# Kernel optimization log

Hardware: AMD Instinct MI355X
Metric: run time of the kernel (lower is better)

The kernel has to match this reference:

```python
import jax, jax.numpy as jnp
import numpy as np


def _quantize(mat):
    # per-row (last-dim) symmetric int8 quantization; scale stored in fp16 like torch
    max_val = (jnp.max(jnp.abs(mat), axis=-1) / 127.0).astype(jnp.float16)
    # torch's .to(int8) truncates toward zero; jnp astype does the same for in-range values
    q = (mat / max_val[..., None].astype(mat.dtype)).astype(jnp.int8)
    return q, max_val


def setup_inputs() -> dict:
    key = jax.random.key(0)
    k1, k2, k3, k4 = jax.random.split(key, 4)
    B, S, D_IN, D_OUT = 4, 2048, 4096, 4096
    x = jax.random.normal(k1, (B, S, D_IN), dtype=jnp.float32)
    origin_weight = jax.random.normal(k2, (D_OUT, D_IN), dtype=jnp.float32) * 0.02
    bias = jax.random.normal(k3, (D_OUT,), dtype=jnp.float32) * 0.01
    act_max = jax.random.normal(k4, (D_IN,), dtype=jnp.float32)
    return {"x": x, "origin_weight": origin_weight, "bias": bias,
            "act_max": act_max, "alpha": 32}


def reference(x, origin_weight, bias, act_max, alpha):
    d_in = act_max.shape[-1]
    # get_unq_idx_topk: top-alpha outlier channels by |act_max|
    _, idx = jax.lax.top_k(jnp.abs(act_max), alpha)          # [alpha]
    t = jnp.ones((d_in,), dtype=origin_weight.dtype).at[idx].set(0)

    # weight decomposition + quantization (done in __init__ in torch)
    weight_q, w_max = _quantize(origin_weight * t)           # [out,in] int8, [out] fp16
    weight_unq = origin_weight[:, idx].T                      # [alpha, out]

    # activation decomposition + per-token quantization
    x_unq = x[..., idx]                                       # [B,S,alpha]
    x_q, x_max = _quantize(x * t.astype(x.dtype))             # [B,S,in] int8, [B,S] fp16

    # simulated MatMulInteger: int8 values multiplied in fp32
    res_q = jnp.matmul(x_q.astype(jnp.float32), weight_q.T.astype(jnp.float32))  # [B,S,out]
    mx = (x_max[..., None] * w_max[None, :]).astype(jnp.float32)                  # [B,S,out]
    res_q = (res_q * mx).astype(x.dtype)

    # fp outlier path
    res_unq = jnp.matmul(x_unq, weight_unq) + bias
    return res_q + res_unq
```

## Files before the change

### kernel.cpp

```cpp
#include <hip/hip_runtime.h>
#include <hip/hip_fp16.h>

typedef __attribute__((ext_vector_type(4)))  int   i32x4;
typedef __attribute__((ext_vector_type(16))) int   i32x16;

#define ALPHA 32
#define BM 256
#define BN 128
#define BK 64


__global__ __launch_bounds__(256) void topk_kernel(const float* __restrict__ act_max,
                                                   int* __restrict__ idx_out,
                                                   unsigned* __restrict__ tbits,
                                                   int K) {
  __shared__ float v[4096];
  __shared__ float rv[4];
  __shared__ int   ri[4];
  __shared__ unsigned bits[128];
  const int t = threadIdx.x;
  for (int i = t; i < K; i += 256) v[i] = fabsf(act_max[i]);
  for (int i = t; i < K / 32; i += 256) bits[i] = 0xFFFFFFFFu;
  __syncthreads();
  for (int sel = 0; sel < ALPHA; ++sel) {
    float bv = -1.f; int bi = 0;
    for (int i = t; i < K; i += 256) {
      float x = v[i];
      if (x > bv) { bv = x; bi = i; }
    }
    for (int m = 1; m < 64; m <<= 1) {
      float ov = __shfl_xor(bv, m);
      int   oi = __shfl_xor(bi, m);
      if (ov > bv || (ov == bv && oi < bi)) { bv = ov; bi = oi; }
    }
    if ((t & 63) == 0) { rv[t >> 6] = bv; ri[t >> 6] = bi; }
    __syncthreads();
    if (t == 0) {
      for (int u = 1; u < 4; ++u)
        if (rv[u] > bv || (rv[u] == bv && ri[u] < bi)) { bv = rv[u]; bi = ri[u]; }
      idx_out[sel] = bi;
      v[bi] = -2.f;
      bits[bi >> 5] &= ~(1u << (bi & 31));
    }
    __syncthreads();
  }
  for (int i = t; i < K / 32; i += 256) tbits[i] = bits[i];
}

__global__ __launch_bounds__(1024) void quant_panel_kernel(
    const float* __restrict__ srcW, const float* __restrict__ srcX,
    const unsigned* __restrict__ tbits, const int* __restrict__ idx,
    signed char* __restrict__ wq, signed char* __restrict__ xq,
    _Float16* __restrict__ wmax, _Float16* __restrict__ xmax,
    float* __restrict__ wuf, float* __restrict__ xuf,
    int npw, int K, int N, int M) {
  const int t = threadIdx.x;
  const int b = blockIdx.x;
  const float* src; signed char* q; _Float16* smax; float* unq; int r0, R;
  if (b < npw) { src = srcW; q = wq; smax = wmax; unq = wuf; r0 = b * 32; R = N; }
  else         { src = srcX; q = xq; smax = xmax; unq = xuf; r0 = (b - npw) * 32; R = M; }
  __shared__ unsigned bits[128];
  __shared__ float wred[8][16];
  __shared__ float scs[8];
  __shared__ signed char qt[8 * 4096];
  const int lane = t & 63, w = t >> 6;
  for (int i = t; i < K / 32; i += 1024) bits[i] = tbits[i];
  __syncthreads();
  const int k0 = t * 4;
  const unsigned bw = bits[k0 >> 5] >> (k0 & 31);
  const bool m0 = bw & 1u, m1 = bw & 2u, m2 = bw & 4u, m3 = bw & 8u;
  const size_t pbase = (size_t)r0 * K;
  for (int g = 0; g < 4; ++g) {
    float4 v[8];
#pragma unroll
    for (int i = 0; i < 8; ++i) {
      float4 x = ((const float4*)(src + (size_t)(r0 + g * 8 + i) * K))[t];
      if (!m0) x.x = 0.f; if (!m1) x.y = 0.f; if (!m2) x.z = 0.f; if (!m3) x.w = 0.f;
      v[i] = x;
      float am = fmaxf(fmaxf(fabsf(x.x), fabsf(x.y)), fmaxf(fabsf(x.z), fabsf(x.w)));
#pragma unroll
      for (int m = 1; m < 64; m <<= 1) am = fmaxf(am, __shfl_xor(am, m));
      if (lane == 0) wred[i][w] = am;
    }
    __syncthreads();
    if (t < 8) {
      float am = wred[t][0];
#pragma unroll
      for (int u = 1; u < 16; ++u) am = fmaxf(am, wred[t][u]);
      _Float16 sh = (_Float16)(am / 127.0f);
      scs[t] = (float)sh;
      smax[r0 + g * 8 + t] = sh;
    }
    __syncthreads();
    const int cc = t >> 2, sub = (t & 3) * 4;
#pragma unroll
    for (int i = 0; i < 8; ++i) {
      const float s = scs[i];
      char4 c;
      c.x = (signed char)(v[i].x / s);
      c.y = (signed char)(v[i].y / s);
      c.z = (signed char)(v[i].z / s);
      c.w = (signed char)(v[i].w / s);
      *(char4*)(qt + cc * 128 + ((i ^ (cc & 7)) << 4) + sub) = c;
    }
    __syncthreads();
#pragma unroll
    for (int i = 0; i < 2; ++i) {
      const int l = i * 1024 + t;
      const int c2 = l >> 3, rl = l & 7;
      int4 d = *(const int4*)(qt + c2 * 128 + ((rl ^ (c2 & 7)) << 4));
      *(int4*)(q + pbase + (size_t)c2 * 512 + (size_t)((g * 8 + rl) << 4)) = d;
    }
    __syncthreads();
  }
  {
    const int j = t >> 5, rl = t & 31;
    unq[(size_t)j * R + r0 + rl] = src[(size_t)(r0 + rl) * K + idx[j]];
  }
}

__device__ __forceinline__ void gld_lds16(const signed char* g, signed char* l) {
  __builtin_amdgcn_global_load_lds(
      (const __attribute__((address_space(1))) void*)g,
      (__attribute__((address_space(3))) void*)l, 16, 0, 0);
}

__global__ __launch_bounds__(256, 2) void gemm_kernel(
    const signed char* __restrict__ xq, const signed char* __restrict__ wq,
    const _Float16* __restrict__ xmax, const _Float16* __restrict__ wmax,
    const float* __restrict__ xuf,
    const float* __restrict__ wuf,
    const float* __restrict__ bias,
    float* __restrict__ out, int M, int N, int K) {
  __shared__ union {
    struct { signed char A[2][BM * BK]; signed char B[2][BN * BK]; } g;
    struct { float xu[ALPHA * BM]; float wu[ALPHA * BN]; } e;
  } sm;
  __shared__ _Float16 xmh[BM];
  __shared__ _Float16 wmh[BN];
  __shared__ float    bl[BN];

  const int t = threadIdx.x;
  const int bid = blockIdx.y * gridDim.x + blockIdx.x;
  const int xcd = bid & 7, loc = bid >> 3;
  const int bxi = xcd * 4 + (loc & 3);
  const int byi = loc >> 2;
  const int bm0 = byi * BM;
  const int bn0 = bxi * BN;
  const int lane = t & 63, w = t >> 6;
  const int wm = w >> 1, wn = w & 1;
  const int hi = lane >> 5, l31 = lane & 31;

  i32x16 acc[4][2] = {};

  const int tp = t >> 7;
  const int to = (t & 127) * 16;
  const signed char* aS = xq + (size_t)bm0 * K + (size_t)tp * 32 * K + to;
  const signed char* bS = wq + (size_t)bn0 * K + (size_t)tp * 32 * K + to;
  signed char* const aD = &sm.g.A[0][0] + t * 16;
  signed char* const bD = &sm.g.B[0][0] + t * 16;
  const size_t PSTR = (size_t)64 * K;

  auto STAGE = [&](int buf, int kt) {
    const size_t ko = (size_t)kt * 2048;
#pragma unroll
    for (int i = 0; i < 4; ++i)
      gld_lds16(aS + (size_t)i * PSTR + ko, aD + buf * (BM * BK) + i * 4096);
#pragma unroll
    for (int i = 0; i < 2; ++i)
      gld_lds16(bS + (size_t)i * PSTR + ko, bD + buf * (BN * BK) + i * 4096);
  };

  STAGE(0, 0);
  const int NT = K >> 6;
  const signed char* const aR0 = &sm.g.A[0][0] + (wm * 4) * 2048 + 16 * lane;
  const signed char* const bR0 = &sm.g.B[0][0] + (wn * 2) * 2048 + 16 * lane;

  for (int kt = 0; kt < NT; ++kt) {
    const int cur = kt & 1;
    asm volatile("s_waitcnt vmcnt(0)" ::: "memory");
    asm volatile("s_barrier" ::: "memory");
    const signed char* aRd = aR0 + cur * (BM * BK);
    const signed char* bRd = bR0 + cur * (BN * BK);
    i32x4 af[2][4], bf[2][2];
#pragma unroll
    for (int ks = 0; ks < 2; ++ks) {
#pragma unroll
      for (int mi = 0; mi < 4; ++mi) af[ks][mi] = *(const i32x4*)(aRd + mi * 2048 + ks * 1024);
#pragma unroll
      for (int ni = 0; ni < 2; ++ni) bf[ks][ni] = *(const i32x4*)(bRd + ni * 2048 + ks * 1024);
    }
    if (kt + 1 < NT) STAGE(cur ^ 1, kt + 1);
    __builtin_amdgcn_s_setprio(1);
#pragma unroll
    for (int ks = 0; ks < 2; ++ks)
#pragma unroll
      for (int mi = 0; mi < 4; ++mi)
#pragma unroll
        for (int ni = 0; ni < 2; ++ni)
          acc[mi][ni] = __builtin_amdgcn_mfma_i32_32x32x32_i8(af[ks][mi], bf[ks][ni], acc[mi][ni], 0, 0, 0);
    __builtin_amdgcn_s_setprio(0);
  }

  __syncthreads();
  {
    const float4* xs = (const float4*)xuf;
    float4* xl = (float4*)sm.e.xu;
#pragma unroll
    for (int i = 0; i < 8; ++i) {
      int p = i * 256 + t;
      int j = p >> 6, r4 = p & 63;
      xl[p] = xs[(size_t)j * (M >> 2) + (bm0 >> 2) + r4];
    }
    const float4* wsrc = (const float4*)wuf;
    float4* wl = (float4*)sm.e.wu;
#pragma unroll
    for (int i = 0; i < 4; ++i) {
      int p = i * 256 + t;
      int j = p >> 5, r4 = p & 31;
      wl[p] = wsrc[(size_t)j * (N >> 2) + (bn0 >> 2) + r4];
    }
    if (t < BM / 2) ((unsigned*)xmh)[t] = ((const unsigned*)(xmax + bm0))[t];
    if (t < BN / 2) ((unsigned*)wmh)[t] = ((const unsigned*)(wmax + bn0))[t];
    if (t < BN / 4) ((float4*)bl)[t] = ((const float4*)(bias + bn0))[t];
  }
  __syncthreads();

  const int c0 = wn * 64 + l31;
  const _Float16 wh0 = wmh[c0], wh1 = wmh[c0 + 32];
  const float bv0 = bl[c0], bv1 = bl[c0 + 32];
  const float* xul = sm.e.xu;
  const float* wul = sm.e.wu;

#pragma unroll
  for (int mi = 0; mi < 4; ++mi) {
    const int rbase = wm * 128 + mi * 32 + 4 * hi;
    float f0[16], f1[16];
#pragma unroll
    for (int r = 0; r < 16; ++r) {
      int row = rbase + (r & 3) + 8 * (r >> 2);
      _Float16 xh = xmh[row];
      float mx0 = (float)(_Float16)(xh * wh0);
      float mx1 = (float)(_Float16)(xh * wh1);
      f0[r] = (float)acc[mi][0][r] * mx0 + bv0;
      f1[r] = (float)acc[mi][1][r] * mx1 + bv1;
    }
#pragma unroll 4
    for (int j = 0; j < ALPHA; ++j) {
      const float4* xrow4 = (const float4*)(xul + j * BM + rbase);
      float wv0 = wul[j * BN + c0];
      float wv1 = wul[j * BN + c0 + 32];
#pragma unroll
      for (int gq = 0; gq < 4; ++gq) {
        float4 xv = xrow4[gq * 2];
        f0[gq * 4 + 0] += xv.x * wv0;  f1[gq * 4 + 0] += xv.x * wv1;
        f0[gq * 4 + 1] += xv.y * wv0;  f1[gq * 4 + 1] += xv.y * wv1;
        f0[gq * 4 + 2] += xv.z * wv0;  f1[gq * 4 + 2] += xv.z * wv1;
        f0[gq * 4 + 3] += xv.w * wv0;  f1[gq * 4 + 3] += xv.w * wv1;
      }
    }
#pragma unroll
    for (int r = 0; r < 16; ++r) {
      int row = bm0 + rbase + (r & 3) + 8 * (r >> 2);
      size_t o = (size_t)row * N + bn0;
      out[o + c0] = f0[r];
      out[o + c0 + 32] = f1[r];
    }
  }
}

extern "C" void kernel_launch(void* const* d_in, const int* in_sizes, int n_in,
                              void* d_out, int out_size, void* d_ws, size_t ws_size,
                              hipStream_t stream) {
  const float* x       = (const float*)d_in[0];
  const float* W       = (const float*)d_in[1];
  const float* bias    = (const float*)d_in[2];
  const float* act_max = (const float*)d_in[3];
  const int K = in_sizes[3];
  const int N = in_sizes[1] / K;
  const int M = in_sizes[0] / K;
  float* out = (float*)d_out;

  char* ws = (char*)d_ws;
  size_t off = 0;
  auto take = [&](size_t b) { char* p = ws + off; off += (b + 255) & ~(size_t)255; return p; };
  signed char* wq  = (signed char*)take((size_t)N * K);
  signed char* xq  = (signed char*)take((size_t)M * K);
  _Float16* wmax   = (_Float16*)take((size_t)N * 2);
  _Float16* xmax   = (_Float16*)take((size_t)M * 2);
  float* wuf       = (float*)take((size_t)ALPHA * N * 4);
  float* xuf       = (float*)take((size_t)ALPHA * M * 4);
  int* idx         = (int*)take(ALPHA * 4);
  unsigned* tbits  = (unsigned*)take((size_t)(K / 32) * 4);

  const int npw = N / 32, npx = M / 32;
  topk_kernel<<<1, 256, 0, stream>>>(act_max, idx, tbits, K);
  quant_panel_kernel<<<npw + npx, 1024, 0, stream>>>(W, x, tbits, idx, wq, xq,
                                                     wmax, xmax, wuf, xuf, npw, K, N, M);
  dim3 grid(N / BN, M / BM);
  gemm_kernel<<<grid, 256, 0, stream>>>(xq, wq, xmax, wmax, xuf, wuf, bias, out, M, N, K);
}
```

Measured before the change: 315.6 us.

## Use triple-buffered GEMM prefetch and 8-row quantization blocks

The GEMM mainloop now keeps three LDS stages, prefetching two k-tiles ahead with a partial vmcnt wait, so global-to-LDS loads overlap further with the MFMA work. The quantization kernel is restructured to 256-thread blocks handling 8 rows each, with one wave per row doing a wave-only max reduction. This removes the cross-wave reductions and extra barriers and launches many more blocks. The cost is more LDS per GEMM block (three stages of A and B), which may limit the intended two blocks per CU.

```diff
diff --git a/kernel.cpp b/kernel.cpp
--- a/kernel.cpp
+++ b/kernel.cpp
@@ -47,75 +47,70 @@
   for (int i = t; i < K / 32; i += 256) tbits[i] = bits[i];
 }
 
-__global__ __launch_bounds__(1024) void quant_panel_kernel(
+__global__ __launch_bounds__(256) void quant8_kernel(
     const float* __restrict__ srcW, const float* __restrict__ srcX,
-    const unsigned* __restrict__ tbits, const int* __restrict__ idx,
+    const unsigned* __restrict__ tbits, const int* __restrict__ idxg,
     signed char* __restrict__ wq, signed char* __restrict__ xq,
     _Float16* __restrict__ wmax, _Float16* __restrict__ xmax,
     float* __restrict__ wuf, float* __restrict__ xuf,
-    int npw, int K, int N, int M) {
-  const int t = threadIdx.x;
+    int nbw, int K, int N, int M) {
+  const int t = threadIdx.x, lane = t & 63, w = t >> 6;
   const int b = blockIdx.x;
   const float* src; signed char* q; _Float16* smax; float* unq; int r0, R;
-  if (b < npw) { src = srcW; q = wq; smax = wmax; unq = wuf; r0 = b * 32; R = N; }
-  else         { src = srcX; q = xq; smax = xmax; unq = xuf; r0 = (b - npw) * 32; R = M; }
+  if (b < nbw) { src = srcW; q = wq; smax = wmax; unq = wuf; r0 = b * 8; R = N; }
+  else         { src = srcX; q = xq; smax = xmax; unq = xuf; r0 = (b - nbw) * 8; R = M; }
   __shared__ unsigned bits[128];
-  __shared__ float wred[8][16];
-  __shared__ float scs[8];
   __shared__ signed char qt[8 * 4096];
-  const int lane = t & 63, w = t >> 6;
-  for (int i = t; i < K / 32; i += 1024) bits[i] = tbits[i];
-  __syncthreads();
-  const int k0 = t * 4;
-  const unsigned bw = bits[k0 >> 5] >> (k0 & 31);
-  const bool m0 = bw & 1u, m1 = bw & 2u, m2 = bw & 4u, m3 = bw & 8u;
-  const size_t pbase = (size_t)r0 * K;
-  for (int g = 0; g < 4; ++g) {
-    float4 v[8];
-#pragma unroll
-    for (int i = 0; i < 8; ++i) {
-      float4 x = ((const float4*)(src + (size_t)(r0 + g * 8 + i) * K))[t];
-      if (!m0) x.x = 0.f; if (!m1) x.y = 0.f; if (!m2) x.z = 0.f; if (!m3) x.w = 0.f;
-      v[i] = x;
-      float am = fmaxf(fmaxf(fabsf(x.x), fabsf(x.y)), fmaxf(fabsf(x.z), fabsf(x.w)));
-#pragma unroll
-      for (int m = 1; m < 64; m <<= 1) am = fmaxf(am, __shfl_xor(am, m));
-      if (lane == 0) wred[i][w] = am;
-    }
-    __syncthreads();
-    if (t < 8) {
-      float am = wred[t][0];
-#pragma unroll
-      for (int u = 1; u < 16; ++u) am = fmaxf(am, wred[t][u]);
-      _Float16 sh = (_Float16)(am / 127.0f);
-      scs[t] = (float)sh;
-      smax[r0 + g * 8 + t] = sh;
-    }
-    __syncthreads();
-    const int cc = t >> 2, sub = (t & 3) * 4;
-#pragma unroll
-    for (int i = 0; i < 8; ++i) {
-      const float s = scs[i];
+  for (int i = t; i < 128; i += 256) bits[i] = tbits[i];
+  __syncthreads();
+  const int shft = (lane & 7) * 4;
+#pragma unroll
+  for (int g = 0; g < 2; ++g) {
+    const int rl = w + 4 * g;
+    const float4* srow = (const float4*)(src + (size_t)(r0 + rl) * K);
+    float4 v[16];
+    float am = 0.f;
+#pragma unroll
+    for (int j = 0; j < 16; ++j) {
+      float4 x = srow[j * 64 + lane];
+      unsigned b4 = bits[j * 8 + (lane >> 3)] >> shft;
+      if (!(b4 & 1u)) x.x = 0.f;
+      if (!(b4 & 2u)) x.y = 0.f;
+      if (!(b4 & 4u)) x.z = 0.f;
+      if (!(b4 & 8u)) x.w = 0.f;
+      v[j] = x;
+      am = fmaxf(am, fmaxf(fmaxf(fabsf(x.x), fabsf(x.y)), fmaxf(fabsf(x.z), fabsf(x.w))));
+    }
+#pragma unroll
+    for (int m = 1; m < 64; m <<= 1) am = fmaxf(am, __shfl_xor(am, m));
+    const _Float16 sh = (_Float16)(am / 127.0f);
+    const float s = (float)sh;
+    if (lane == 0) smax[r0 + rl] = sh;
+    signed char* row = qt + rl * 4096;
+#pragma unroll
+    for (int j = 0; j < 16; ++j) {
+      float4 x = v[j];
       char4 c;
-      c.x = (signed char)(v[i].x / s);
-      c.y = (signed char)(v[i].y / s);
-      c.z = (signed char)(v[i].z / s);
-      c.w = (signed char)(v[i].w / s);
-      *(char4*)(qt + cc * 128 + ((i ^ (cc & 7)) << 4) + sub) = c;
-    }
-    __syncthreads();
-#pragma unroll
-    for (int i = 0; i < 2; ++i) {
-      const int l = i * 1024 + t;
-      const int c2 = l >> 3, rl = l & 7;
-      int4 d = *(const int4*)(qt + c2 * 128 + ((rl ^ (c2 & 7)) << 4));
-      *(int4*)(q + pbase + (size_t)c2 * 512 + (size_t)((g * 8 + rl) << 4)) = d;
-    }
-    __syncthreads();
+      c.x = (signed char)(x.x / s);
+      c.y = (signed char)(x.y / s);
+      c.z = (signed char)(x.z / s);
+      c.w = (signed char)(x.w / s);
+      const int c2 = j * 16 + (lane >> 2);
+      *(char4*)(row + ((c2 ^ rl) << 4) + (lane & 3) * 4) = c;
+    }
+  }
+  __syncthreads();
+  const size_t pbase = (size_t)(r0 >> 5) * 32 * K + (size_t)(r0 & 31) * 16;
+#pragma unroll
+  for (int i = 0; i < 8; ++i) {
+    const int s2 = i * 256 + t;
+    const int c2 = s2 >> 3, rl = s2 & 7;
+    int4 d = *(const int4*)(qt + rl * 4096 + ((c2 ^ rl) << 4));
+    *(int4*)(q + pbase + (size_t)c2 * 512 + rl * 16) = d;
   }
   {
-    const int j = t >> 5, rl = t & 31;
-    unq[(size_t)j * R + r0 + rl] = src[(size_t)(r0 + rl) * K + idx[j]];
+    const int j = t >> 3, rl = t & 7;
+    unq[(size_t)j * R + r0 + rl] = src[(size_t)(r0 + rl) * K + idxg[j]];
   }
 }
 
@@ -133,7 +128,7 @@
     const float* __restrict__ bias,
     float* __restrict__ out, int M, int N, int K) {
   __shared__ union {
-    struct { signed char A[2][BM * BK]; signed char B[2][BN * BK]; } g;
+    struct { signed char A[3][BM * BK]; signed char B[3][BN * BK]; } g;
     struct { float xu[ALPHA * BM]; float wu[ALPHA * BN]; } e;
   } sm;
   __shared__ _Float16 xmh[BM];
@@ -171,13 +166,40 @@
       gld_lds16(bS + (size_t)i * PSTR + ko, bD + buf * (BN * BK) + i * 4096);
   };
 
+  const int NT = K >> 6;
   STAGE(0, 0);
-  const int NT = K >> 6;
+  STAGE(1, 1);
   const signed char* const aR0 = &sm.g.A[0][0] + (wm * 4) * 2048 + 16 * lane;
   const signed char* const bR0 = &sm.g.B[0][0] + (wn * 2) * 2048 + 16 * lane;
 
-  for (int kt = 0; kt < NT; ++kt) {
-    const int cur = kt & 1;
+  int cur = 0, st = 2;
+  for (int kt = 0; kt < NT - 1; ++kt) {
+    asm volatile("s_waitcnt vmcnt(6)" ::: "memory");
+    asm volatile("s_barrier" ::: "memory");
+    const signed char* aRd = aR0 + cur * (BM * BK);
+    const signed char* bRd = bR0 + cur * (BN * BK);
+    i32x4 af[2][4], bf[2][2];
+#pragma unroll
+    for (int ks = 0; ks < 2; ++ks) {
+#pragma unroll
+      for (int mi = 0; mi < 4; ++mi) af[ks][mi] = *(const i32x4*)(aRd + mi * 2048 + ks * 1024);
+#pragma unroll
+      for (int ni = 0; ni < 2; ++ni) bf[ks][ni] = *(const i32x4*)(bRd + ni * 2048 + ks * 1024);
+    }
+    if (kt + 2 < NT) STAGE(st, kt + 2);
+    __builtin_amdgcn_s_setprio(1);
+#pragma unroll
+    for (int ks = 0; ks < 2; ++ks)
+#pragma unroll
+      for (int mi = 0; mi < 4; ++mi)
+#pragma unroll
+        for (int ni = 0; ni < 2; ++ni)
+          acc[mi][ni] = __builtin_amdgcn_mfma_i32_32x32x32_i8(af[ks][mi], bf[ks][ni], acc[mi][ni], 0, 0, 0);
+    __builtin_amdgcn_s_setprio(0);
+    if (++cur == 3) cur = 0;
+    if (++st == 3) st = 0;
+  }
+  {
     asm volatile("s_waitcnt vmcnt(0)" ::: "memory");
     asm volatile("s_barrier" ::: "memory");
     const signed char* aRd = aR0 + cur * (BM * BK);
@@ -190,7 +212,6 @@
 #pragma unroll
       for (int ni = 0; ni < 2; ++ni) bf[ks][ni] = *(const i32x4*)(bRd + ni * 2048 + ks * 1024);
     }
-    if (kt + 1 < NT) STAGE(cur ^ 1, kt + 1);
     __builtin_amdgcn_s_setprio(1);
 #pragma unroll
     for (int ks = 0; ks < 2; ++ks)
@@ -293,10 +314,10 @@
   int* idx         = (int*)take(ALPHA * 4);
   unsigned* tbits  = (unsigned*)take((size_t)(K / 32) * 4);
 
-  const int npw = N / 32, npx = M / 32;
+  const int nbw = N / 8, nbx = M / 8;
   topk_kernel<<<1, 256, 0, stream>>>(act_max, idx, tbits, K);
-  quant_panel_kernel<<<npw + npx, 1024, 0, stream>>>(W, x, tbits, idx, wq, xq,
-                                                     wmax, xmax, wuf, xuf, npw, K, N, M);
+  quant8_kernel<<<nbw + nbx, 256, 0, stream>>>(W, x, tbits, idx, wq, xq,
+                                               wmax, xmax, wuf, xuf, nbw, K, N, M);
   dim3 grid(N / BN, M / BM);
   gemm_kernel<<<grid, 256, 0, stream>>>(xq, wq, xmax, wmax, xuf, wuf, bias, out, M, N, K);
 }
```

Result: faster. 276.8 us (-12.3%).
